# Optimization experiments

Hardware: AMD Instinct MI355X
Metric: run time of the kernel (lower is better)

Reference implementation:

```python
import jax, jax.numpy as jnp
import numpy as np

DIM = 1024
N_HEADS = 16
HEAD_DIM = DIM // N_HEADS


def setup_inputs() -> dict:
    key = jax.random.key(0)
    kx, kq, kk, kv, ko = jax.random.split(key, 5)
    B, S = 2, 2048
    scale = 1.0 / np.sqrt(DIM)
    return {
        "x": jax.random.normal(kx, (B, S, DIM), dtype=jnp.float32),
        "Wq": jax.random.normal(kq, (DIM, DIM), dtype=jnp.float32) * scale,
        "Wk": jax.random.normal(kk, (DIM, DIM), dtype=jnp.float32) * scale,
        "Wv": jax.random.normal(kv, (DIM, DIM), dtype=jnp.float32) * scale,
        "Wo": jax.random.normal(ko, (DIM, DIM), dtype=jnp.float32) * scale,
    }


def rotate_half(x):
    x1, x2 = jnp.split(x, 2, axis=-1)
    return jnp.concatenate([-x2, x1], axis=-1)


def rope_freqs(seq_len, dim):
    inv_freq = 1.0 / (10000.0 ** (jnp.arange(0, dim, 2, dtype=jnp.float32) / dim))
    t = jnp.arange(seq_len, dtype=jnp.float32)
    freqs = jnp.einsum('i,j->ij', t, inv_freq)  # [S, dim/2]
    return jnp.concatenate([freqs, freqs], axis=-1)  # [S, dim]


def apply_rotary(x, freqs):
    # x: [B, H, S, Dh], freqs: [S, Dh]
    cos = jnp.cos(freqs)[None, None]
    sin = jnp.sin(freqs)[None, None]
    return x * cos + rotate_half(x) * sin


def reference(x, Wq, Wk, Wv, Wo):
    B, S, D = x.shape
    H, Dh = N_HEADS, HEAD_DIM
    # nn.Linear(dim, dim, bias=False): y = x @ W.T
    q = (x @ Wq.T).reshape(B, S, H, Dh).transpose(0, 2, 1, 3)
    k = (x @ Wk.T).reshape(B, S, H, Dh).transpose(0, 2, 1, 3)
    v = (x @ Wv.T).reshape(B, S, H, Dh).transpose(0, 2, 1, 3)
    freqs = rope_freqs(S, Dh)
    q = apply_rotary(q, freqs)
    k = apply_rotary(k, freqs)
    attn = jnp.einsum('bhqd,bhkd->bhqk', q, k) / jnp.sqrt(jnp.float32(Dh))
    attn = jax.nn.softmax(attn, axis=-1)
    out = jnp.einsum('bhqk,bhkd->bhqd', attn, v)
    out = out.transpose(0, 2, 1, 3).reshape(B, S, D)
    return out @ Wo.T
```

## Files before the change

### kernel.cpp

```cpp
#include <hip/hip_runtime.h>
#include <hip/hip_bf16.h>

#define NB 2
#define NS 2048
#define ND 1024
#define NH 16
#define NDH 64
#define NM 4096

typedef __bf16 bf16;
typedef __bf16 bf16x8 __attribute__((ext_vector_type(8)));
typedef __bf16 bf16x4 __attribute__((ext_vector_type(4)));
typedef float f32x4 __attribute__((ext_vector_type(4)));

#define ASYNC16(g, l) __builtin_amdgcn_global_load_lds( \
    (const __attribute__((address_space(1))) void*)(g), \
    (__attribute__((address_space(3))) void*)(l), 16, 0, 0)

__global__ __launch_bounds__(256) void convert_kernel(
    const float* __restrict__ x,
    const float* __restrict__ wq, const float* __restrict__ wk,
    const float* __restrict__ wv, const float* __restrict__ wo,
    bf16* __restrict__ xb, bf16* __restrict__ wb) {
  int i = blockIdx.x * 256 + threadIdx.x;
  const int n_x4 = (NM * ND) / 4;
  const int n_w4 = (ND * ND) / 4;
  float4 v;
  bf16* dst;
  if (i < n_x4) {
    v = ((const float4*)x)[i];
    dst = xb + (size_t)i * 4;
  } else {
    int j = i - n_x4;
    int w = j / n_w4;
    int o = j - w * n_w4;
    const float* W = (w == 0) ? wq : (w == 1) ? wk : (w == 2) ? wv : wo;
    v = ((const float4*)W)[o];
    dst = wb + (size_t)w * (ND * ND) + (size_t)o * 4;
  }
  bf16x4 o4;
  o4[0] = (bf16)v.x; o4[1] = (bf16)v.y; o4[2] = (bf16)v.z; o4[3] = (bf16)v.w;
  *(bf16x4*)dst = o4;
}

template <int EPI>
__global__ __launch_bounds__(256) void gemm_bt(
    const bf16* __restrict__ A, const bf16* __restrict__ Bmat,
    void* __restrict__ Cbase, int Mm, int Nn, int Kk) {
  __shared__ bf16 As[128 * 64];
  __shared__ bf16 Bs[128 * 64];
  const int t = threadIdx.x;
  const int lane = t & 63, w = t >> 6;
  const int wr = w >> 1, wc = w & 1;
  const int bm = blockIdx.y * 128;
  const int bn = blockIdx.x * 128;
  const bf16* Bz = Bmat + (size_t)blockIdx.z * Nn * Kk;

  f32x4 acc[4][4];
#pragma unroll
  for (int i = 0; i < 4; ++i)
#pragma unroll
    for (int j = 0; j < 4; ++j) acc[i][j] = (f32x4){0.f, 0.f, 0.f, 0.f};

  for (int kt = 0; kt < Kk / 64; ++kt) {
    __syncthreads();
#pragma unroll
    for (int i = 0; i < 4; ++i) {
      int c = w * 64 + lane + i * 256;
      int row = c >> 3;
      int js = (c & 7) ^ (row & 7);
      ASYNC16(A + (size_t)(bm + row) * Kk + kt * 64 + js * 8, As + c * 8);
      ASYNC16(Bz + (size_t)(bn + row) * Kk + kt * 64 + js * 8, Bs + c * 8);
    }
    __syncthreads();
#pragma unroll
    for (int ks = 0; ks < 2; ++ks) {
      const int kb = ks * 64 + (lane >> 4) * 16;
      bf16x8 af[4], bfr[4];
#pragma unroll
      for (int i = 0; i < 4; ++i) {
        int ra = wr * 64 + i * 16 + (lane & 15);
        af[i] = *(const bf16x8*)((const char*)As + ra * 128 + (kb ^ ((ra & 7) << 4)));
        int rb = wc * 64 + i * 16 + (lane & 15);
        bfr[i] = *(const bf16x8*)((const char*)Bs + rb * 128 + (kb ^ ((rb & 7) << 4)));
      }
#pragma unroll
      for (int i = 0; i < 4; ++i)
#pragma unroll
        for (int j = 0; j < 4; ++j)
          acc[i][j] = __builtin_amdgcn_mfma_f32_16x16x32_bf16(af[i], bfr[j], acc[i][j], 0, 0, 0);
    }
  }

  const int row0 = bm + wr * 64;
  const int col0 = bn + wc * 64;
#pragma unroll
  for (int i = 0; i < 4; ++i)
#pragma unroll
    for (int j = 0; j < 4; ++j) {
      int r = row0 + i * 16 + (lane >> 4) * 4;
      int ccol = col0 + j * 16 + (lane & 15);
#pragma unroll
      for (int q = 0; q < 4; ++q) {
        size_t idx = (size_t)(r + q) * Nn + ccol;
        if (EPI == 0)
          ((bf16*)Cbase)[(size_t)blockIdx.z * Mm * Nn + idx] = (bf16)acc[i][j][q];
        else
          ((float*)Cbase)[idx] = acc[i][j][q];
      }
    }
}

__global__ __launch_bounds__(256) void rope_kernel(
    const bf16* __restrict__ qraw, const bf16* __restrict__ kraw,
    bf16* __restrict__ Qr, bf16* __restrict__ Kr) {
  int t = blockIdx.x * 256 + threadIdx.x;
  int which = t >> 21;
  int r = t & ((1 << 21) - 1);
  int d = r & 31;
  int s = (r >> 5) & 2047;
  int bh = r >> 16;
  int b = bh >> 4, h = bh & 15;
  const bf16* src = which ? kraw : qraw;
  bf16* dst = which ? Kr : Qr;
  size_t si = ((size_t)(b * NS + s)) * ND + h * NDH + d;
  float x1 = (float)src[si];
  float x2 = (float)src[si + 32];
  float invf = exp2f(-13.28771237954945f * ((float)d * (1.0f / 32.0f)));
  float f = (float)s * invf;
  float sn, c;
  sincosf(f, &sn, &c);
  float scale = which ? 1.0f : 0.125f;
  size_t di = ((size_t)bh * NS + s) * NDH + d;
  dst[di]      = (bf16)((x1 * c - x2 * sn) * scale);
  dst[di + 32] = (bf16)((x2 * c + x1 * sn) * scale);
}

__global__ __launch_bounds__(256) void transv_kernel(
    const bf16* __restrict__ vraw, bf16* __restrict__ VT) {
  __shared__ bf16 tl[64][65];
  int s0 = blockIdx.x * 64;
  int bh = blockIdx.y;
  int b = bh >> 4, h = bh & 15;
  int t = threadIdx.x;
#pragma unroll
  for (int i = 0; i < 4; ++i) {
    int row = (t >> 4) + i * 16;
    int d4 = (t & 15) * 4;
    *(bf16x4*)&tl[row][d4] =
        *(const bf16x4*)&vraw[((size_t)(b * NS + s0 + row)) * ND + h * NDH + d4];
  }
  __syncthreads();
#pragma unroll
  for (int i = 0; i < 4; ++i) {
    int dr = (t >> 4) + i * 16;
    int s4 = (t & 15) * 4;
    bf16x4 o;
    o[0] = tl[s4 + 0][dr]; o[1] = tl[s4 + 1][dr];
    o[2] = tl[s4 + 2][dr]; o[3] = tl[s4 + 3][dr];
    *(bf16x4*)&VT[((size_t)(bh * NDH + dr)) * NS + s0 + s4] = o;
  }
}

__global__ __launch_bounds__(256) void attn_kernel(
    const bf16* __restrict__ Qr, const bf16* __restrict__ Kr,
    const bf16* __restrict__ VT, bf16* __restrict__ out) {
  __shared__ bf16 Ks[64 * 64];
  __shared__ bf16 Vs[64 * 64];
  __shared__ bf16 Ps[4 * 16 * 64];
  const int t = threadIdx.x, lane = t & 63, w = t >> 6;
  const int bh = blockIdx.y;
  const int q0 = blockIdx.x * 64 + w * 16;
  const bf16* Qbase = Qr + ((size_t)bh * NS + q0) * NDH;

  bf16x8 qf[2];
  {
    int qr = lane & 15;
    int ko = (lane >> 4) * 8;
    qf[0] = *(const bf16x8*)(Qbase + (size_t)qr * NDH + ko);
    qf[1] = *(const bf16x8*)(Qbase + (size_t)qr * NDH + 32 + ko);
  }

  f32x4 o[4];
#pragma unroll
  for (int i = 0; i < 4; ++i) o[i] = (f32x4){0.f, 0.f, 0.f, 0.f};
  float mrow[4], lrow[4];
#pragma unroll
  for (int j = 0; j < 4; ++j) { mrow[j] = -1e30f; lrow[j] = 0.f; }

  for (int kt = 0; kt < NS / 64; ++kt) {
    __syncthreads();
#pragma unroll
    for (int i = 0; i < 2; ++i) {
      int c = w * 64 + lane + i * 256;
      int row = c >> 3;
      int js = (c & 7) ^ (row & 7);
      ASYNC16(Kr + ((size_t)bh * NS + kt * 64 + row) * NDH + js * 8, Ks + c * 8);
      ASYNC16(VT + ((size_t)bh * NDH + row) * NS + kt * 64 + js * 8, Vs + c * 8);
    }
    __syncthreads();

    f32x4 sc[4];
#pragma unroll
    for (int nf = 0; nf < 4; ++nf) sc[nf] = (f32x4){0.f, 0.f, 0.f, 0.f};
#pragma unroll
    for (int ks = 0; ks < 2; ++ks) {
      const int kb = ks * 64 + (lane >> 4) * 16;
#pragma unroll
      for (int nf = 0; nf < 4; ++nf) {
        int rk = nf * 16 + (lane & 15);
        bf16x8 kf = *(const bf16x8*)((const char*)Ks + rk * 128 + (kb ^ ((rk & 7) << 4)));
        sc[nf] = __builtin_amdgcn_mfma_f32_16x16x32_bf16(qf[ks], kf, sc[nf], 0, 0, 0);
      }
    }

    float pv[4][4], scl[4];
#pragma unroll
    for (int j = 0; j < 4; ++j) {
      float mx = fmaxf(fmaxf(sc[0][j], sc[1][j]), fmaxf(sc[2][j], sc[3][j]));
#pragma unroll
      for (int off = 1; off < 16; off <<= 1) mx = fmaxf(mx, __shfl_xor(mx, off, 64));
      float mnew = fmaxf(mrow[j], mx);
      scl[j] = __expf(mrow[j] - mnew);
      float sum = 0.f;
#pragma unroll
      for (int nf = 0; nf < 4; ++nf) {
        float p = __expf(sc[nf][j] - mnew);
        pv[nf][j] = p;
        sum += p;
      }
#pragma unroll
      for (int off = 1; off < 16; off <<= 1) sum += __shfl_xor(sum, off, 64);
      lrow[j] = lrow[j] * scl[j] + sum;
      mrow[j] = mnew;
    }

#pragma unroll
    for (int j = 0; j < 4; ++j) {
      int r = (lane >> 4) * 4 + j;
      char* base = (char*)Ps + w * 2048 + r * 128;
#pragma unroll
      for (int nf = 0; nf < 4; ++nf) {
        int key = nf * 16 + (lane & 15);
        *(bf16*)(base + ((key * 2) ^ ((r & 7) << 4))) = (bf16)pv[nf][j];
      }
    }
#pragma unroll
    for (int df = 0; df < 4; ++df)
#pragma unroll
      for (int j = 0; j < 4; ++j) o[df][j] *= scl[j];

#pragma unroll
    for (int ks = 0; ks < 2; ++ks) {
      const int kb = ks * 64 + (lane >> 4) * 16;
      int rp = lane & 15;
      bf16x8 pf = *(const bf16x8*)((const char*)Ps + w * 2048 + rp * 128 + (kb ^ ((rp & 7) << 4)));
#pragma unroll
      for (int df = 0; df < 4; ++df) {
        int rv = df * 16 + (lane & 15);
        bf16x8 vf = *(const bf16x8*)((const char*)Vs + rv * 128 + (kb ^ ((rv & 7) << 4)));
        o[df] = __builtin_amdgcn_mfma_f32_16x16x32_bf16(pf, vf, o[df], 0, 0, 0);
      }
    }
  }

  const int b = bh >> 4, h = bh & 15;
#pragma unroll
  for (int df = 0; df < 4; ++df)
#pragma unroll
    for (int j = 0; j < 4; ++j) {
      int srow = q0 + (lane >> 4) * 4 + j;
      int d = df * 16 + (lane & 15);
      out[((size_t)(b * NS + srow)) * ND + h * NDH + d] = (bf16)(o[df][j] / lrow[j]);
    }
}

extern "C" void kernel_launch(void* const* d_in, const int* in_sizes, int n_in,
                              void* d_out, int out_size, void* d_ws, size_t ws_size,
                              hipStream_t stream) {
  const float* x  = (const float*)d_in[0];
  const float* wq = (const float*)d_in[1];
  const float* wk = (const float*)d_in[2];
  const float* wv = (const float*)d_in[3];
  const float* wo = (const float*)d_in[4];
  char* ws = (char*)d_ws;
  bf16* xb   = (bf16*)(ws);
  bf16* wb   = (bf16*)(ws + (8u << 20));
  bf16* qkv  = (bf16*)(ws + (16u << 20));
  bf16* Qr   = (bf16*)(ws + (40u << 20));
  bf16* Kr   = (bf16*)(ws + (48u << 20));
  bf16* VT   = (bf16*)(ws + (56u << 20));
  bf16* attn = (bf16*)(ws + (64u << 20));
  float* out = (float*)d_out;

  convert_kernel<<<8192, 256, 0, stream>>>(x, wq, wk, wv, wo, xb, wb);
  gemm_bt<0><<<dim3(8, 32, 3), 256, 0, stream>>>(xb, wb, (void*)qkv, NM, ND, ND);
  rope_kernel<<<16384, 256, 0, stream>>>(qkv, qkv + (size_t)NM * ND, Qr, Kr);
  transv_kernel<<<dim3(32, 32), 256, 0, stream>>>(qkv + (size_t)2 * NM * ND, VT);
  attn_kernel<<<dim3(32, 32), 256, 0, stream>>>(Qr, Kr, VT, attn);
  gemm_bt<1><<<dim3(8, 32, 1), 256, 0, stream>>>(attn, wb + 3 * ND * ND, (void*)out, NM, ND, ND);
}
```

Measured before the change: 263.0 us.

## Fuse RoPE into QKV GEMM and rewrite attention with 32x32 MFMA double buffering

Replaces the standalone RoPE kernel with a precomputed cos/sin table applied in the QKV GEMM epilogue, which removes one full read and write of Q/K. The attention kernel is rewritten to use 32x32x16 MFMA with 128-query blocks and double-buffered K/V LDS loads. It keeps P in registers through cross-lane shuffles instead of staging it in LDS, and only rescales the running max when it grows by more than a threshold. Blocks are also remapped with a swizzled order. The lazy rescale and the register shuffle layout add numerical and correctness risk.

```diff
diff --git a/kernel.cpp b/kernel.cpp
--- a/kernel.cpp
+++ b/kernel.cpp
@@ -12,10 +12,17 @@
 typedef __bf16 bf16x8 __attribute__((ext_vector_type(8)));
 typedef __bf16 bf16x4 __attribute__((ext_vector_type(4)));
 typedef float f32x4 __attribute__((ext_vector_type(4)));
+typedef float f32x16 __attribute__((ext_vector_type(16)));
 
 #define ASYNC16(g, l) __builtin_amdgcn_global_load_lds( \
     (const __attribute__((address_space(1))) void*)(g), \
     (__attribute__((address_space(3))) void*)(l), 16, 0, 0)
+
+static __device__ __forceinline__ unsigned cvt_pk_bf16(float a, float b) {
+  unsigned r;
+  asm("v_cvt_pk_bf16_f32 %0, %1, %2" : "=v"(r) : "v"(a), "v"(b));
+  return r;
+}
 
 __global__ __launch_bounds__(256) void convert_kernel(
     const float* __restrict__ x,
@@ -43,10 +50,20 @@
   *(bf16x4*)dst = o4;
 }
 
-template <int EPI>
-__global__ __launch_bounds__(256) void gemm_bt(
+__global__ __launch_bounds__(256) void tab_kernel(float2* __restrict__ tab) {
+  int t = blockIdx.x * 256 + threadIdx.x;
+  int s = t >> 5, d = t & 31;
+  float invf = exp2f(-0.4152410118609203f * (float)d);
+  float f = (float)s * invf;
+  float sn, cs;
+  sincosf(f, &sn, &cs);
+  tab[t] = make_float2(cs, sn);
+}
+
+__global__ __launch_bounds__(256) void gemm_qkv(
     const bf16* __restrict__ A, const bf16* __restrict__ Bmat,
-    void* __restrict__ Cbase, int Mm, int Nn, int Kk) {
+    bf16* __restrict__ Qr, bf16* __restrict__ Kr, bf16* __restrict__ vraw,
+    const float2* __restrict__ tab) {
   __shared__ bf16 As[128 * 64];
   __shared__ bf16 Bs[128 * 64];
   const int t = threadIdx.x;
@@ -54,7 +71,8 @@
   const int wr = w >> 1, wc = w & 1;
   const int bm = blockIdx.y * 128;
   const int bn = blockIdx.x * 128;
-  const bf16* Bz = Bmat + (size_t)blockIdx.z * Nn * Kk;
+  const int z = blockIdx.z;
+  const bf16* Bz = Bmat + (size_t)z * ND * ND;
 
   f32x4 acc[4][4];
 #pragma unroll
@@ -62,15 +80,15 @@
 #pragma unroll
     for (int j = 0; j < 4; ++j) acc[i][j] = (f32x4){0.f, 0.f, 0.f, 0.f};
 
-  for (int kt = 0; kt < Kk / 64; ++kt) {
+  for (int kt = 0; kt < ND / 64; ++kt) {
     __syncthreads();
 #pragma unroll
     for (int i = 0; i < 4; ++i) {
       int c = w * 64 + lane + i * 256;
       int row = c >> 3;
       int js = (c & 7) ^ (row & 7);
-      ASYNC16(A + (size_t)(bm + row) * Kk + kt * 64 + js * 8, As + c * 8);
-      ASYNC16(Bz + (size_t)(bn + row) * Kk + kt * 64 + js * 8, Bs + c * 8);
+      ASYNC16(A + (size_t)(bm + row) * ND + kt * 64 + js * 8, As + c * 8);
+      ASYNC16(Bz + (size_t)(bn + row) * ND + kt * 64 + js * 8, Bs + c * 8);
     }
     __syncthreads();
 #pragma unroll
@@ -94,6 +112,89 @@
 
   const int row0 = bm + wr * 64;
   const int col0 = bn + wc * 64;
+  if (z == 2) {
+#pragma unroll
+    for (int i = 0; i < 4; ++i)
+#pragma unroll
+      for (int j = 0; j < 4; ++j) {
+        int r = row0 + i * 16 + (lane >> 4) * 4;
+        int ccol = col0 + j * 16 + (lane & 15);
+#pragma unroll
+        for (int q = 0; q < 4; ++q)
+          vraw[(size_t)(r + q) * ND + ccol] = (bf16)acc[i][j][q];
+      }
+  } else {
+    bf16* dst = z ? Kr : Qr;
+    const float qs = z ? 1.0f : 0.125f;
+    const int h = col0 >> 6;
+    const int ln15 = lane & 15;
+#pragma unroll
+    for (int i = 0; i < 4; ++i)
+#pragma unroll
+      for (int j = 0; j < 2; ++j)
+#pragma unroll
+        for (int q = 0; q < 4; ++q) {
+          int r = row0 + i * 16 + (lane >> 4) * 4 + q;
+          int b = r >> 11, s = r & (NS - 1);
+          int d1 = j * 16 + ln15;
+          float2 tc = tab[s * 32 + d1];
+          float x1 = acc[i][j][q], x2 = acc[i][j + 2][q];
+          size_t base = ((size_t)((b * NH + h) * NS + s)) * NDH;
+          dst[base + d1]      = (bf16)((x1 * tc.x - x2 * tc.y) * qs);
+          dst[base + d1 + 32] = (bf16)((x2 * tc.x + x1 * tc.y) * qs);
+        }
+  }
+}
+
+__global__ __launch_bounds__(256) void gemm_out(
+    const bf16* __restrict__ A, const bf16* __restrict__ Bmat,
+    float* __restrict__ Cout) {
+  __shared__ bf16 As[128 * 64];
+  __shared__ bf16 Bs[128 * 64];
+  const int t = threadIdx.x;
+  const int lane = t & 63, w = t >> 6;
+  const int wr = w >> 1, wc = w & 1;
+  const int bm = blockIdx.y * 128;
+  const int bn = blockIdx.x * 128;
+
+  f32x4 acc[4][4];
+#pragma unroll
+  for (int i = 0; i < 4; ++i)
+#pragma unroll
+    for (int j = 0; j < 4; ++j) acc[i][j] = (f32x4){0.f, 0.f, 0.f, 0.f};
+
+  for (int kt = 0; kt < ND / 64; ++kt) {
+    __syncthreads();
+#pragma unroll
+    for (int i = 0; i < 4; ++i) {
+      int c = w * 64 + lane + i * 256;
+      int row = c >> 3;
+      int js = (c & 7) ^ (row & 7);
+      ASYNC16(A + (size_t)(bm + row) * ND + kt * 64 + js * 8, As + c * 8);
+      ASYNC16(Bmat + (size_t)(bn + row) * ND + kt * 64 + js * 8, Bs + c * 8);
+    }
+    __syncthreads();
+#pragma unroll
+    for (int ks = 0; ks < 2; ++ks) {
+      const int kb = ks * 64 + (lane >> 4) * 16;
+      bf16x8 af[4], bfr[4];
+#pragma unroll
+      for (int i = 0; i < 4; ++i) {
+        int ra = wr * 64 + i * 16 + (lane & 15);
+        af[i] = *(const bf16x8*)((const char*)As + ra * 128 + (kb ^ ((ra & 7) << 4)));
+        int rb = wc * 64 + i * 16 + (lane & 15);
+        bfr[i] = *(const bf16x8*)((const char*)Bs + rb * 128 + (kb ^ ((rb & 7) << 4)));
+      }
+#pragma unroll
+      for (int i = 0; i < 4; ++i)
+#pragma unroll
+        for (int j = 0; j < 4; ++j)
+          acc[i][j] = __builtin_amdgcn_mfma_f32_16x16x32_bf16(af[i], bfr[j], acc[i][j], 0, 0, 0);
+    }
+  }
+
+  const int row0 = bm + wr * 64;
+  const int col0 = bn + wc * 64;
 #pragma unroll
   for (int i = 0; i < 4; ++i)
 #pragma unroll
@@ -101,39 +202,9 @@
       int r = row0 + i * 16 + (lane >> 4) * 4;
       int ccol = col0 + j * 16 + (lane & 15);
 #pragma unroll
-      for (int q = 0; q < 4; ++q) {
-        size_t idx = (size_t)(r + q) * Nn + ccol;
-        if (EPI == 0)
-          ((bf16*)Cbase)[(size_t)blockIdx.z * Mm * Nn + idx] = (bf16)acc[i][j][q];
-        else
-          ((float*)Cbase)[idx] = acc[i][j][q];
-      }
-    }
-}
-
-__global__ __launch_bounds__(256) void rope_kernel(
-    const bf16* __restrict__ qraw, const bf16* __restrict__ kraw,
-    bf16* __restrict__ Qr, bf16* __restrict__ Kr) {
-  int t = blockIdx.x * 256 + threadIdx.x;
-  int which = t >> 21;
-  int r = t & ((1 << 21) - 1);
-  int d = r & 31;
-  int s = (r >> 5) & 2047;
-  int bh = r >> 16;
-  int b = bh >> 4, h = bh & 15;
-  const bf16* src = which ? kraw : qraw;
-  bf16* dst = which ? Kr : Qr;
-  size_t si = ((size_t)(b * NS + s)) * ND + h * NDH + d;
-  float x1 = (float)src[si];
-  float x2 = (float)src[si + 32];
-  float invf = exp2f(-13.28771237954945f * ((float)d * (1.0f / 32.0f)));
-  float f = (float)s * invf;
-  float sn, c;
-  sincosf(f, &sn, &c);
-  float scale = which ? 1.0f : 0.125f;
-  size_t di = ((size_t)bh * NS + s) * NDH + d;
-  dst[di]      = (bf16)((x1 * c - x2 * sn) * scale);
-  dst[di + 32] = (bf16)((x2 * c + x1 * sn) * scale);
+      for (int q = 0; q < 4; ++q)
+        Cout[(size_t)(r + q) * ND + ccol] = acc[i][j][q];
+    }
 }
 
 __global__ __launch_bounds__(256) void transv_kernel(
@@ -165,114 +236,132 @@
 __global__ __launch_bounds__(256) void attn_kernel(
     const bf16* __restrict__ Qr, const bf16* __restrict__ Kr,
     const bf16* __restrict__ VT, bf16* __restrict__ out) {
-  __shared__ bf16 Ks[64 * 64];
-  __shared__ bf16 Vs[64 * 64];
-  __shared__ bf16 Ps[4 * 16 * 64];
+  __shared__ bf16 Ks[2][64 * 64];
+  __shared__ bf16 Vs[2][64 * 64];
   const int t = threadIdx.x, lane = t & 63, w = t >> 6;
-  const int bh = blockIdx.y;
-  const int q0 = blockIdx.x * 64 + w * 16;
-  const bf16* Qbase = Qr + ((size_t)bh * NS + q0) * NDH;
-
-  bf16x8 qf[2];
+  const int hi = lane >> 5, ln = lane & 31;
+  int wg = blockIdx.x;
+  int sw = (wg & 7) * 64 + (wg >> 3);
+  const int qb = sw & 15, bh = sw >> 4;
+  const int q0 = qb * 128 + w * 32;
+
+  bf16x8 qv[4];
   {
-    int qr = lane & 15;
-    int ko = (lane >> 4) * 8;
-    qf[0] = *(const bf16x8*)(Qbase + (size_t)qr * NDH + ko);
-    qf[1] = *(const bf16x8*)(Qbase + (size_t)qr * NDH + 32 + ko);
-  }
-
-  f32x4 o[4];
-#pragma unroll
-  for (int i = 0; i < 4; ++i) o[i] = (f32x4){0.f, 0.f, 0.f, 0.f};
-  float mrow[4], lrow[4];
-#pragma unroll
-  for (int j = 0; j < 4; ++j) { mrow[j] = -1e30f; lrow[j] = 0.f; }
-
+    const bf16* Qb = Qr + ((size_t)bh * NS + q0 + ln) * NDH + hi * 8;
+#pragma unroll
+    for (int c = 0; c < 4; ++c) qv[c] = *(const bf16x8*)(Qb + c * 16);
+  }
+
+  f32x16 O0, O1;
+#pragma unroll
+  for (int r = 0; r < 16; ++r) { O0[r] = 0.f; O1[r] = 0.f; }
+  float m = -1e30f, l = 0.f;
+
+#pragma unroll
+  for (int i = 0; i < 2; ++i) {
+    int ch = t + i * 256;
+    int row = ch >> 3, js = (ch & 7) ^ (row & 7);
+    ASYNC16(Kr + ((size_t)bh * NS + row) * NDH + js * 8, &Ks[0][ch * 8]);
+    ASYNC16(VT + ((size_t)bh * NDH + row) * NS + js * 8, &Vs[0][ch * 8]);
+  }
+  __syncthreads();
+
+  int cur = 0;
   for (int kt = 0; kt < NS / 64; ++kt) {
-    __syncthreads();
-#pragma unroll
-    for (int i = 0; i < 2; ++i) {
-      int c = w * 64 + lane + i * 256;
-      int row = c >> 3;
-      int js = (c & 7) ^ (row & 7);
-      ASYNC16(Kr + ((size_t)bh * NS + kt * 64 + row) * NDH + js * 8, Ks + c * 8);
-      ASYNC16(VT + ((size_t)bh * NDH + row) * NS + kt * 64 + js * 8, Vs + c * 8);
-    }
-    __syncthreads();
-
-    f32x4 sc[4];
-#pragma unroll
-    for (int nf = 0; nf < 4; ++nf) sc[nf] = (f32x4){0.f, 0.f, 0.f, 0.f};
-#pragma unroll
-    for (int ks = 0; ks < 2; ++ks) {
-      const int kb = ks * 64 + (lane >> 4) * 16;
-#pragma unroll
-      for (int nf = 0; nf < 4; ++nf) {
-        int rk = nf * 16 + (lane & 15);
-        bf16x8 kf = *(const bf16x8*)((const char*)Ks + rk * 128 + (kb ^ ((rk & 7) << 4)));
-        sc[nf] = __builtin_amdgcn_mfma_f32_16x16x32_bf16(qf[ks], kf, sc[nf], 0, 0, 0);
+    if (kt + 1 < NS / 64) {
+      int nb = cur ^ 1;
+#pragma unroll
+      for (int i = 0; i < 2; ++i) {
+        int ch = t + i * 256;
+        int row = ch >> 3, js = (ch & 7) ^ (row & 7);
+        ASYNC16(Kr + ((size_t)bh * NS + (kt + 1) * 64 + row) * NDH + js * 8, &Ks[nb][ch * 8]);
+        ASYNC16(VT + ((size_t)bh * NDH + row) * NS + (kt + 1) * 64 + js * 8, &Vs[nb][ch * 8]);
       }
     }
-
-    float pv[4][4], scl[4];
-#pragma unroll
-    for (int j = 0; j < 4; ++j) {
-      float mx = fmaxf(fmaxf(sc[0][j], sc[1][j]), fmaxf(sc[2][j], sc[3][j]));
-#pragma unroll
-      for (int off = 1; off < 16; off <<= 1) mx = fmaxf(mx, __shfl_xor(mx, off, 64));
-      float mnew = fmaxf(mrow[j], mx);
-      scl[j] = __expf(mrow[j] - mnew);
-      float sum = 0.f;
-#pragma unroll
-      for (int nf = 0; nf < 4; ++nf) {
-        float p = __expf(sc[nf][j] - mnew);
-        pv[nf][j] = p;
-        sum += p;
-      }
-#pragma unroll
-      for (int off = 1; off < 16; off <<= 1) sum += __shfl_xor(sum, off, 64);
-      lrow[j] = lrow[j] * scl[j] + sum;
-      mrow[j] = mnew;
-    }
-
-#pragma unroll
-    for (int j = 0; j < 4; ++j) {
-      int r = (lane >> 4) * 4 + j;
-      char* base = (char*)Ps + w * 2048 + r * 128;
-#pragma unroll
-      for (int nf = 0; nf < 4; ++nf) {
-        int key = nf * 16 + (lane & 15);
-        *(bf16*)(base + ((key * 2) ^ ((r & 7) << 4))) = (bf16)pv[nf][j];
-      }
-    }
-#pragma unroll
-    for (int df = 0; df < 4; ++df)
-#pragma unroll
-      for (int j = 0; j < 4; ++j) o[df][j] *= scl[j];
-
-#pragma unroll
-    for (int ks = 0; ks < 2; ++ks) {
-      const int kb = ks * 64 + (lane >> 4) * 16;
-      int rp = lane & 15;
-      bf16x8 pf = *(const bf16x8*)((const char*)Ps + w * 2048 + rp * 128 + (kb ^ ((rp & 7) << 4)));
-#pragma unroll
-      for (int df = 0; df < 4; ++df) {
-        int rv = df * 16 + (lane & 15);
-        bf16x8 vf = *(const bf16x8*)((const char*)Vs + rv * 128 + (kb ^ ((rv & 7) << 4)));
-        o[df] = __builtin_amdgcn_mfma_f32_16x16x32_bf16(pf, vf, o[df], 0, 0, 0);
-      }
-    }
-  }
-
+    const char* Kb = (const char*)Ks[cur];
+    const char* Vb = (const char*)Vs[cur];
+
+    f32x16 s0, s1;
+#pragma unroll
+    for (int r = 0; r < 16; ++r) { s0[r] = 0.f; s1[r] = 0.f; }
+#pragma unroll
+    for (int c = 0; c < 4; ++c) {
+      int ko = c * 32 + hi * 16;
+      int r0 = ln, r1 = 32 + ln;
+      bf16x8 k0 = *(const bf16x8*)(Kb + r0 * 128 + (ko ^ ((r0 & 7) << 4)));
+      bf16x8 k1 = *(const bf16x8*)(Kb + r1 * 128 + (ko ^ ((r1 & 7) << 4)));
+      s0 = __builtin_amdgcn_mfma_f32_32x32x16_bf16(k0, qv[c], s0, 0, 0, 0);
+      s1 = __builtin_amdgcn_mfma_f32_32x32x16_bf16(k1, qv[c], s1, 0, 0, 0);
+    }
+
+    float pmax = s0[0];
+#pragma unroll
+    for (int r = 1; r < 16; ++r) pmax = fmaxf(pmax, s0[r]);
+#pragma unroll
+    for (int r = 0; r < 16; ++r) pmax = fmaxf(pmax, s1[r]);
+    pmax = fmaxf(pmax, __shfl_xor(pmax, 32, 64));
+
+    if (!__all(pmax - m <= 8.0f)) {
+      float mnew = fmaxf(m, pmax);
+      float scl = __expf(m - mnew);
+      m = mnew; l *= scl;
+#pragma unroll
+      for (int r = 0; r < 16; ++r) { O0[r] *= scl; O1[r] *= scl; }
+    }
+
+    float p0[16], p1[16], sum = 0.f;
+#pragma unroll
+    for (int r = 0; r < 16; ++r) { p0[r] = __expf(s0[r] - m); sum += p0[r]; }
+#pragma unroll
+    for (int r = 0; r < 16; ++r) { p1[r] = __expf(s1[r] - m); sum += p1[r]; }
+    sum += __shfl_xor(sum, 32, 64);
+    l += sum;
+
+    unsigned u0[8], u1[8], x0[8], x1[8];
+#pragma unroll
+    for (int g = 0; g < 4; ++g) {
+      u0[g]     = cvt_pk_bf16(p0[4 * g],     p0[4 * g + 1]);
+      u1[g]     = cvt_pk_bf16(p0[4 * g + 2], p0[4 * g + 3]);
+      u0[4 + g] = cvt_pk_bf16(p1[4 * g],     p1[4 * g + 1]);
+      u1[4 + g] = cvt_pk_bf16(p1[4 * g + 2], p1[4 * g + 3]);
+    }
+#pragma unroll
+    for (int g = 0; g < 8; ++g) {
+      x0[g] = __shfl_xor(u0[g], 32, 64);
+      x1[g] = __shfl_xor(u1[g], 32, 64);
+    }
+
+#pragma unroll
+    for (int c = 0; c < 4; ++c) {
+      int base = (c >> 1) * 4 + (c & 1) * 2;
+      union { unsigned u[4]; bf16x8 v; } pa;
+      pa.u[0] = hi ? x0[base + 1] : u0[base];
+      pa.u[1] = hi ? x1[base + 1] : u1[base];
+      pa.u[2] = hi ? u0[base + 1] : x0[base];
+      pa.u[3] = hi ? u1[base + 1] : x1[base];
+      int ko = c * 32 + hi * 16;
+      int rv0 = ln, rv1 = 32 + ln;
+      bf16x8 v0 = *(const bf16x8*)(Vb + rv0 * 128 + (ko ^ ((rv0 & 7) << 4)));
+      bf16x8 v1 = *(const bf16x8*)(Vb + rv1 * 128 + (ko ^ ((rv1 & 7) << 4)));
+      O0 = __builtin_amdgcn_mfma_f32_32x32x16_bf16(pa.v, v0, O0, 0, 0, 0);
+      O1 = __builtin_amdgcn_mfma_f32_32x32x16_bf16(pa.v, v1, O1, 0, 0, 0);
+    }
+
+    __syncthreads();
+    cur ^= 1;
+  }
+
+  float rl = 1.0f / l;
   const int b = bh >> 4, h = bh & 15;
 #pragma unroll
-  for (int df = 0; df < 4; ++df)
-#pragma unroll
-    for (int j = 0; j < 4; ++j) {
-      int srow = q0 + (lane >> 4) * 4 + j;
-      int d = df * 16 + (lane & 15);
-      out[((size_t)(b * NS + srow)) * ND + h * NDH + d] = (bf16)(o[df][j] / lrow[j]);
-    }
+  for (int r = 0; r < 16; ++r) {
+    int q = (r & 3) + 8 * (r >> 2) + 4 * hi;
+    float rlq = __shfl(rl, q, 64);
+    int s = q0 + q;
+    size_t base = ((size_t)(b * NS + s)) * ND + h * NDH + ln;
+    out[base]      = (bf16)(O0[r] * rlq);
+    out[base + 32] = (bf16)(O1[r] * rlq);
+  }
 }
 
 extern "C" void kernel_launch(void* const* d_in, const int* in_sizes, int n_in,
@@ -284,19 +373,20 @@
   const float* wv = (const float*)d_in[3];
   const float* wo = (const float*)d_in[4];
   char* ws = (char*)d_ws;
-  bf16* xb   = (bf16*)(ws);
-  bf16* wb   = (bf16*)(ws + (8u << 20));
-  bf16* qkv  = (bf16*)(ws + (16u << 20));
-  bf16* Qr   = (bf16*)(ws + (40u << 20));
-  bf16* Kr   = (bf16*)(ws + (48u << 20));
-  bf16* VT   = (bf16*)(ws + (56u << 20));
-  bf16* attn = (bf16*)(ws + (64u << 20));
-  float* out = (float*)d_out;
+  bf16* xb    = (bf16*)(ws);
+  bf16* wb    = (bf16*)(ws + (8u << 20));
+  bf16* vraw  = (bf16*)(ws + (16u << 20));
+  bf16* Qr    = (bf16*)(ws + (24u << 20));
+  bf16* Kr    = (bf16*)(ws + (32u << 20));
+  bf16* VT    = (bf16*)(ws + (40u << 20));
+  bf16* attnb = (bf16*)(ws + (48u << 20));
+  float2* tab = (float2*)(ws + (56u << 20));
+  float* out  = (float*)d_out;
 
   convert_kernel<<<8192, 256, 0, stream>>>(x, wq, wk, wv, wo, xb, wb);
-  gemm_bt<0><<<dim3(8, 32, 3), 256, 0, stream>>>(xb, wb, (void*)qkv, NM, ND, ND);
-  rope_kernel<<<16384, 256, 0, stream>>>(qkv, qkv + (size_t)NM * ND, Qr, Kr);
-  transv_kernel<<<dim3(32, 32), 256, 0, stream>>>(qkv + (size_t)2 * NM * ND, VT);
-  attn_kernel<<<dim3(32, 32), 256, 0, stream>>>(Qr, Kr, VT, attn);
-  gemm_bt<1><<<dim3(8, 32, 1), 256, 0, stream>>>(attn, wb + 3 * ND * ND, (void*)out, NM, ND, ND);
-}
+  tab_kernel<<<256, 256, 0, stream>>>(tab);
+  gemm_qkv<<<dim3(8, 32, 3), 256, 0, stream>>>(xb, wb, Qr, Kr, vraw, tab);
+  transv_kernel<<<dim3(32, 32), 256, 0, stream>>>(vraw, VT);
+  attn_kernel<<<dim3(512), 256, 0, stream>>>(Qr, Kr, VT, attnb);
+  gemm_out<<<dim3(8, 32), 256, 0, stream>>>(attnb, wb + 3 * ND * ND, out);
+}
```

Measured after the change: 216.0 us. -17.9%, faster.
